# Performance work log

Measured on AMD Instinct MI355X. Metric: run time of the kernel, lower is better.

## Reference

```python
import jax, jax.numpy as jnp
import numpy as np

D_MODEL = 768
HIDDEN = 2048  # round(768*8/3)=2048, already a multiple of 64
N_EXPERTS = 8
ALPHA = 0.05  # load_balance_alpha


def setup_inputs() -> dict:
    key = jax.random.key(0)
    k0, k1, k2, k3, k4 = jax.random.split(key, 5)
    x = jax.random.normal(k0, (2, 2048, D_MODEL), dtype=jnp.float32)
    wg_w = jax.random.normal(k1, (N_EXPERTS, D_MODEL), dtype=jnp.float32) * 0.02
    wg_b = jnp.zeros((N_EXPERTS,), dtype=jnp.float32)
    Wu = jax.random.normal(k2, (N_EXPERTS, D_MODEL, HIDDEN), dtype=jnp.float32) * 0.02
    Wv = jax.random.normal(k3, (N_EXPERTS, D_MODEL, HIDDEN), dtype=jnp.float32) * 0.02
    Wd = jax.random.normal(k4, (N_EXPERTS, HIDDEN, D_MODEL), dtype=jnp.float32) * 0.02
    return {"x": x, "wg_w": wg_w, "wg_b": wg_b, "Wu": Wu, "Wv": Wv, "Wd": Wd}


def reference(x, wg_w, wg_b, Wu, Wv, Wd):
    b, t, d = x.shape
    xf = x.reshape(b * t, d)  # [N, d]

    # ---- Top1Router (eval mode: temp=1, no noise, z_loss_coef=0) ----
    logits = xf @ wg_w.T + wg_b            # [N, E]
    probs = jax.nn.softmax(logits, axis=-1)
    top1_idx = jnp.argmax(logits, axis=-1)  # [N]
    top1_p = jnp.take_along_axis(probs, top1_idx[:, None], axis=1)[:, 0]  # [N]

    # aux loss: me and ce computed under no_grad in the torch source -> stop_gradient
    one_hot = jax.nn.one_hot(top1_idx, N_EXPERTS, dtype=probs.dtype)
    me = jax.lax.stop_gradient(one_hot.mean(axis=0))   # [E]
    ce = jax.lax.stop_gradient(probs.mean(axis=0))     # [E]
    aux = ALPHA * N_EXPERTS * jnp.sum(me * ce)

    # ---- Dropless dispatch: per-expert masked SwiGLU, combined with top1 gate ----
    gate = top1_p[:, None]  # [N, 1]
    y = jnp.zeros_like(xf)
    for e in range(N_EXPERTS):
        mask = (top1_idx == e)[:, None]            # [N, 1]
        xe = jnp.where(mask, xf, 0.0)              # zero-out non-routed tokens (no biases -> exact)
        u = xe @ Wu[e]                              # [N, H]
        v = xe @ Wv[e]                              # [N, H]
        ye = (jax.nn.silu(u) * v) @ Wd[e]           # [N, d]
        y = y + jnp.where(mask, ye * gate, 0.0)
    return y.reshape(b, t, d), aux
```

## Files before the change

### kernel.cpp

```cpp
#include <hip/hip_runtime.h>
#include <cstdint>
#include <cstddef>

#define TOK 4096
#define DM 768
#define HID 2048
#define NE 8

typedef __attribute__((ext_vector_type(8))) short bf16x8;
typedef __attribute__((ext_vector_type(4))) float f32x4;

#define ASYNC16(GP, LP) \
  __builtin_amdgcn_global_load_lds((__attribute__((address_space(1))) void*)(GP), \
                                   (__attribute__((address_space(3))) void*)(LP), 16, 0, 0)

__device__ __forceinline__ unsigned short f2bf(float f) {
  unsigned int u = __float_as_uint(f);
  u += 0x7FFF + ((u >> 16) & 1);
  return (unsigned short)(u >> 16);
}
__device__ __forceinline__ unsigned int pack2(float a, float b) {
  return (unsigned)f2bf(a) | ((unsigned)f2bf(b) << 16);
}
__device__ __forceinline__ int padded_off(const int* counts, int e) {
  int o = 0;
  for (int i = 0; i < e; ++i) o += (counts[i] + 127) & ~127;
  return o;
}

__global__ __launch_bounds__(256)
void k_gate(const float* __restrict__ x, const float* __restrict__ wgw,
            const float* __restrict__ wgb,
            int* __restrict__ eidx, float* __restrict__ gatep,
            float* __restrict__ cepart)
{
  __shared__ float ce_loc[4][NE];
  const int lane = threadIdx.x & 63;
  const int w = threadIdx.x >> 6;
  const int t = blockIdx.x * 4 + w;
  float acc[NE];
#pragma unroll
  for (int e = 0; e < NE; ++e) acc[e] = 0.f;
  const float* xr = x + (size_t)t * DM;
#pragma unroll
  for (int j = 0; j < DM / 64; ++j) {
    float xv = xr[j * 64 + lane];
#pragma unroll
    for (int e = 0; e < NE; ++e) acc[e] += xv * wgw[e * DM + j * 64 + lane];
  }
#pragma unroll
  for (int e = 0; e < NE; ++e) {
    float v = acc[e];
#pragma unroll
    for (int off = 32; off >= 1; off >>= 1) v += __shfl_xor(v, off);
    acc[e] = v + wgb[e];
  }
  float mx = acc[0]; int ai = 0;
#pragma unroll
  for (int e = 1; e < NE; ++e) if (acc[e] > mx) { mx = acc[e]; ai = e; }
  float p[NE]; float se = 0.f;
#pragma unroll
  for (int e = 0; e < NE; ++e) { p[e] = expf(acc[e] - mx); se += p[e]; }
  float inv = 1.f / se;
  if (lane == 0) {
#pragma unroll
    for (int e = 0; e < NE; ++e) ce_loc[w][e] = p[e] * inv;
    eidx[t] = ai;
    gatep[t] = p[ai] * inv;
  }
  __syncthreads();
  if (threadIdx.x < NE) {
    float s = ce_loc[0][threadIdx.x] + ce_loc[1][threadIdx.x]
            + ce_loc[2][threadIdx.x] + ce_loc[3][threadIdx.x];
    cepart[blockIdx.x * NE + threadIdx.x] = s;
  }
}

__global__ __launch_bounds__(256)
void k_convert(const float* __restrict__ Wu, const float* __restrict__ Wv,
               const float* __restrict__ Wd,
               unsigned short* __restrict__ wub, unsigned short* __restrict__ wvb,
               unsigned short* __restrict__ wdb)
{
  const int cb = blockIdx.x;
  const int seg = cb / 1536;
  const int r = cb % 1536;
  const int e = r / 192;
  const int rem = r % 192;
  const float* W;
  unsigned short* blobbase;
  int N, nt, kt2;
  if (seg < 2) {
    N = HID; nt = rem / 12; kt2 = rem % 12;
    W = ((seg == 0) ? Wu : Wv) + (size_t)e * DM * HID;
    blobbase = ((seg == 0) ? wub : wvb) + ((size_t)((e * 16 + nt) * 24) << 12);
  } else {
    N = DM; nt = rem / 32; kt2 = rem % 32;
    W = Wd + (size_t)e * HID * DM;
    blobbase = wdb + ((size_t)((e * 6 + nt) * 64) << 12);
  }
  const int t = threadIdx.x;
  const int n4 = t & 31, ko8 = t >> 5;
  const float* src = W + (size_t)(kt2 * 64 + ko8 * 8) * N + nt * 128 + n4 * 4;
  float4 f[8];
#pragma unroll
  for (int j = 0; j < 8; ++j) f[j] = *(const float4*)(src + (size_t)j * N);
  const int kt = kt2 * 2 + (ko8 >> 2), ko = ko8 & 3;
  unsigned short* dst = blobbase + ((size_t)kt << 12) + (size_t)(ko * 128 + n4 * 4) * 8;
#pragma unroll
  for (int i = 0; i < 4; ++i) {
    uint4 u;
    u.x = pack2(((const float*)&f[0])[i], ((const float*)&f[1])[i]);
    u.y = pack2(((const float*)&f[2])[i], ((const float*)&f[3])[i]);
    u.z = pack2(((const float*)&f[4])[i], ((const float*)&f[5])[i]);
    u.w = pack2(((const float*)&f[6])[i], ((const float*)&f[7])[i]);
    *(uint4*)(dst + i * 8) = u;
  }
}

__global__ __launch_bounds__(256)
void k_count(const int* __restrict__ eidx, const float* __restrict__ gatep,
             const float* __restrict__ cepart,
             int* __restrict__ prow_arr, int* __restrict__ tlist,
             float* __restrict__ gate_b, int* __restrict__ counts_g,
             float* __restrict__ aux_out)
{
  __shared__ int hist[256][NE];
  __shared__ float fs[256][NE];
  __shared__ int po_s[NE], cnt_s[NE];
  const int tid = threadIdx.x;
  int own[NE], v[NE], el[16];
#pragma unroll
  for (int e = 0; e < NE; ++e) own[e] = 0;
#pragma unroll
  for (int j = 0; j < 16; ++j) {
    el[j] = eidx[tid * 16 + j];
#pragma unroll
    for (int e = 0; e < NE; ++e) own[e] += (el[j] == e) ? 1 : 0;
  }
#pragma unroll
  for (int e = 0; e < NE; ++e) { v[e] = own[e]; hist[tid][e] = v[e]; }
  __syncthreads();
  for (int st = 1; st < 256; st <<= 1) {
    int add[NE];
#pragma unroll
    for (int e = 0; e < NE; ++e) add[e] = (tid >= st) ? hist[tid - st][e] : 0;
    __syncthreads();
#pragma unroll
    for (int e = 0; e < NE; ++e) { v[e] += add[e]; hist[tid][e] = v[e]; }
    __syncthreads();
  }
  if (tid == 0) {
    int o = 0;
#pragma unroll
    for (int e = 0; e < NE; ++e) {
      int c = hist[255][e];
      cnt_s[e] = c; counts_g[e] = c; po_s[e] = o;
      o += (c + 127) & ~127;
    }
  }
  __syncthreads();
  int run[NE];
#pragma unroll
  for (int e = 0; e < NE; ++e) run[e] = po_s[e] + v[e] - own[e];
#pragma unroll
  for (int j = 0; j < 16; ++j) {
    const int t = tid * 16 + j;
    const int e = el[j];
    int p = 0;
#pragma unroll
    for (int k = 0; k < NE; ++k) if (e == k) p = run[k]++;
    prow_arr[t] = p;
    tlist[p] = t;
    gate_b[p] = gatep[t];
  }
  float s[NE];
#pragma unroll
  for (int e = 0; e < NE; ++e) s[e] = 0.f;
  for (int bb = tid; bb < 1024; bb += 256)
#pragma unroll
    for (int e = 0; e < NE; ++e) s[e] += cepart[bb * NE + e];
#pragma unroll
  for (int e = 0; e < NE; ++e) fs[tid][e] = s[e];
  __syncthreads();
  for (int st = 128; st > 0; st >>= 1) {
    if (tid < st)
#pragma unroll
      for (int e = 0; e < NE; ++e) fs[tid][e] += fs[tid + st][e];
    __syncthreads();
  }
  if (tid == 0) {
    float aux = 0.f;
    for (int e = 0; e < NE; ++e)
      aux += ((float)cnt_s[e] / 4096.f) * (fs[0][e] / 4096.f);
    aux_out[0] = 0.05f * 8.f * aux;
  }
}

__global__ __launch_bounds__(256)
void k2_scatter_zero(const float* __restrict__ x, const int* __restrict__ prow_arr,
                     unsigned short* __restrict__ xb, float* __restrict__ y)
{
  const int b = blockIdx.x;
  if (b < 1024) {
    const int lane = threadIdx.x & 63;
    const int w = threadIdx.x >> 6;
    const int t = b * 4 + w;
    const int prow = prow_arr[t];
    const float4* src4 = (const float4*)(x + (size_t)t * DM);
    uint2* dst = (uint2*)(xb + (size_t)prow * DM);
#pragma unroll
    for (int c = 0; c < 3; ++c) {
      float4 v = src4[lane + c * 64];
      uint2 d; d.x = pack2(v.x, v.y); d.y = pack2(v.z, v.w);
      dst[lane + c * 64] = d;
    }
  } else {
    float4* y4 = (float4*)y;
    const int base = (b - 1024) * 1536 + threadIdx.x;
#pragma unroll
    for (int c = 0; c < 6; ++c) {
      float4 z; z.x = 0.f; z.y = 0.f; z.z = 0.f; z.w = 0.f;
      y4[base + c * 256] = z;
    }
  }
}

__global__ __launch_bounds__(256, 2)
void k_ffn1(const unsigned short* __restrict__ wub, const unsigned short* __restrict__ wvb,
            const unsigned short* __restrict__ xb, const float* __restrict__ gate_b,
            const int* __restrict__ counts, unsigned short* __restrict__ h)
{
  const int e = blockIdx.z;
  const int Me = counts[e];
  const int tm = blockIdx.y;
  if (tm * 128 >= Me) return;
  const int tn = blockIdx.x;
  const int prowbase = padded_off(counts, e) + tm * 128;

  __shared__ __align__(16) unsigned short Sh[24576];

  const int tid = threadIdx.x;
  const int lane = tid & 63;
  const int wv_ = tid >> 6;
  const int wm = wv_ >> 1, wn = wv_ & 1;
  const int wu_id = __builtin_amdgcn_readfirstlane(wv_);

  f32x4 accU[4][4], accV[4][4];
#pragma unroll
  for (int i = 0; i < 4; ++i)
#pragma unroll
    for (int j = 0; j < 4; ++j)
#pragma unroll
      for (int k = 0; k < 4; ++k) { accU[i][j][k] = 0.f; accV[i][j][k] = 0.f; }

  const char* BuBase = (const char*)wub + ((size_t)((e * 16 + tn) * 24) << 13);
  const char* BvBase = (const char*)wvb + ((size_t)((e * 16 + tn) * 24) << 13);

  const char* sp[12]; size_t stp[12];
#pragma unroll
  for (int c2 = 0; c2 < 12; ++c2) {
    const int c = wu_id * 12 + c2;
    const int reg = c >> 3, i8 = c & 7;
    const int sub = (reg >= 3);
    const int rr = (reg >= 3) ? reg - 3 : reg;
    const int s = i8 * 64 + lane;
    if (rr == 0) {
      int m = s >> 2, ko = (s & 3) ^ (m & 3);
      sp[c2] = (const char*)xb + (size_t)(prowbase + m) * (DM * 2) + sub * 64 + ko * 16;
      stp[c2] = 128;
    } else {
      int n = s >> 2, ko = (s & 3) ^ (n & 3);
      const char* base = (rr == 1) ? BuBase : BvBase;
      sp[c2] = base + (size_t)sub * 8192 + (size_t)(ko * 128 + n) * 16;
      stp[c2] = 16384;
    }
  }
  const int lc = lane & 15, q = lane >> 4;

  for (int kt2 = 0; kt2 < 12; ++kt2) {
#pragma unroll
    for (int c2 = 0; c2 < 12; ++c2) {
      ASYNC16(sp[c2], (char*)Sh + (unsigned)((wu_id * 12 + c2) * 1024));
      sp[c2] += stp[c2];
    }
    __syncthreads();
#pragma unroll
    for (int sub = 0; sub < 2; ++sub) {
      const int sb = sub * 12288;
      bf16x8 a[4], bu[4], bv[4];
#pragma unroll
      for (int i = 0; i < 4; ++i) {
        int m = wm * 64 + i * 16 + lc;
        a[i] = *(const bf16x8*)&Sh[sb + (m * 4 + (q ^ (m & 3))) * 8];
      }
#pragma unroll
      for (int j = 0; j < 4; ++j) {
        int n = wn * 64 + j * 16 + lc;
        int slb = (n * 4 + (q ^ (n & 3))) * 8;
        bu[j] = *(const bf16x8*)&Sh[sb + 4096 + slb];
        bv[j] = *(const bf16x8*)&Sh[sb + 8192 + slb];
      }
#pragma unroll
      for (int i = 0; i < 4; ++i)
#pragma unroll
        for (int j = 0; j < 4; ++j) {
          accU[i][j] = __builtin_amdgcn_mfma_f32_16x16x32_bf16(a[i], bu[j], accU[i][j], 0, 0, 0);
          accV[i][j] = __builtin_amdgcn_mfma_f32_16x16x32_bf16(a[i], bv[j], accV[i][j], 0, 0, 0);
        }
    }
    __syncthreads();
  }
  const int colbase = tn * 128 + wn * 64;
  const int rlane = (lane >> 4) * 4;
  const int clane = lane & 15;
#pragma unroll
  for (int i = 0; i < 4; ++i) {
#pragma unroll
    for (int r = 0; r < 4; ++r) {
      int rowIn = wm * 64 + i * 16 + rlane + r;
      if (tm * 128 + rowIn < Me) {
        int prow = prowbase + rowIn;
        float g = gate_b[prow];
        unsigned short* hp = h + (size_t)prow * HID + colbase + clane;
#pragma unroll
        for (int j = 0; j < 4; ++j) {
          float u_ = accU[i][j][r];
          float v_ = accV[i][j][r];
          float sv = u_ / (1.f + expf(-u_));
          hp[j * 16] = f2bf(sv * v_ * g);
        }
      }
    }
  }
}

__global__ __launch_bounds__(256, 2)
void k_ffn2(const unsigned short* __restrict__ wdb, const unsigned short* __restrict__ h,
            const int* __restrict__ counts, const int* __restrict__ tlist,
            float* __restrict__ y)
{
  const int z = blockIdx.z;
  const int e = z >> 2, split = z & 3;
  const int Me = counts[e];
  const int tm = blockIdx.y;
  if (tm * 128 >= Me) return;
  const int tn = blockIdx.x;
  const int prowbase = padded_off(counts, e) + tm * 128;

  __shared__ __align__(16) unsigned short Sh[16384];

  const int tid = threadIdx.x;
  const int lane = tid & 63;
  const int wv_ = tid >> 6;
  const int wm = wv_ >> 1, wn = wv_ & 1;
  const int wu_id = __builtin_amdgcn_readfirstlane(wv_);

  f32x4 acc[4][4];
#pragma unroll
  for (int i = 0; i < 4; ++i)
#pragma unroll
    for (int j = 0; j < 4; ++j)
#pragma unroll
      for (int k = 0; k < 4; ++k) acc[i][j][k] = 0.f;

  const char* BdBase = (const char*)wdb + ((size_t)((e * 6 + tn) * 64) << 13);

  const char* sp[8]; size_t stp[8];
#pragma unroll
  for (int c2 = 0; c2 < 8; ++c2) {
    const int c = wu_id * 8 + c2;
    const int reg = c >> 3, i8 = c & 7;
    const int sub = reg >> 1;
    const int s = i8 * 64 + lane;
    if ((reg & 1) == 0) {
      int m = s >> 2, ko = (s & 3) ^ (m & 3);
      sp[c2] = (const char*)h + (size_t)(prowbase + m) * (HID * 2)
             + split * 1024 + sub * 64 + ko * 16;
      stp[c2] = 128;
    } else {
      int n = s >> 2, ko = (s & 3) ^ (n & 3);
      sp[c2] = BdBase + (size_t)(split * 16 + sub) * 8192 + (size_t)(ko * 128 + n) * 16;
      stp[c2] = 16384;
    }
  }
  const int lc = lane & 15, q = lane >> 4;

  for (int kti = 0; kti < 8; ++kti) {
#pragma unroll
    for (int c2 = 0; c2 < 8; ++c2) {
      ASYNC16(sp[c2], (char*)Sh + (unsigned)((wu_id * 8 + c2) * 1024));
      sp[c2] += stp[c2];
    }
    __syncthreads();
#pragma unroll
    for (int sub = 0; sub < 2; ++sub) {
      const int sb = sub * 8192;
      bf16x8 a[4], bfr[4];
#pragma unroll
      for (int i = 0; i < 4; ++i) {
        int m = wm * 64 + i * 16 + lc;
        a[i] = *(const bf16x8*)&Sh[sb + (m * 4 + (q ^ (m & 3))) * 8];
      }
#pragma unroll
      for (int j = 0; j < 4; ++j) {
        int n = wn * 64 + j * 16 + lc;
        bfr[j] = *(const bf16x8*)&Sh[sb + 4096 + (n * 4 + (q ^ (n & 3))) * 8];
      }
#pragma unroll
      for (int i = 0; i < 4; ++i)
#pragma unroll
        for (int j = 0; j < 4; ++j)
          acc[i][j] = __builtin_amdgcn_mfma_f32_16x16x32_bf16(a[i], bfr[j], acc[i][j], 0, 0, 0);
    }
    __syncthreads();
  }
  const int colbase = tn * 128 + wn * 64;
  const int rlane = (lane >> 4) * 4;
  const int clane = lane & 15;
#pragma unroll
  for (int i = 0; i < 4; ++i) {
#pragma unroll
    for (int r = 0; r < 4; ++r) {
      int rowIn = wm * 64 + i * 16 + rlane + r;
      if (tm * 128 + rowIn < Me) {
        int tok = tlist[prowbase + rowIn];
        float* yp = y + (size_t)tok * DM + colbase + clane;
#pragma unroll
        for (int j = 0; j < 4; ++j) atomicAdd(&yp[j * 16], acc[i][j][r]);
      }
    }
  }
}

extern "C" void kernel_launch(void* const* d_in, const int* in_sizes, int n_in,
                              void* d_out, int out_size, void* d_ws, size_t ws_size,
                              hipStream_t stream)
{
  const float* x   = (const float*)d_in[0];
  const float* wgw = (const float*)d_in[1];
  const float* wgb = (const float*)d_in[2];
  const float* Wu  = (const float*)d_in[3];
  const float* Wv  = (const float*)d_in[4];
  const float* Wd  = (const float*)d_in[5];
  float* out = (float*)d_out;

  char* ws = (char*)d_ws;
  int*   counts = (int*)(ws + 0);
  int*   eidx   = (int*)(ws + 256);
  float* gatep  = (float*)(ws + 16640);
  int*   prow   = (int*)(ws + 33024);
  float* cepart = (float*)(ws + 49408);
  int*   tlist  = (int*)(ws + 82176);
  float* gate_b = (float*)(ws + 102656);
  unsigned short* xb  = (unsigned short*)(ws + 123136);
  unsigned short* h   = (unsigned short*)(ws + 7987456);
  unsigned short* wub = (unsigned short*)(ws + 28958976);
  unsigned short* wvb = (unsigned short*)(ws + 54124800);
  unsigned short* wdb = (unsigned short*)(ws + 79290624);

  k_gate<<<1024, 256, 0, stream>>>(x, wgw, wgb, eidx, gatep, cepart);
  k_convert<<<4608, 256, 0, stream>>>(Wu, Wv, Wd, wub, wvb, wdb);
  k_count<<<1, 256, 0, stream>>>(eidx, gatep, cepart, prow, tlist, gate_b,
                                 counts, out + (size_t)TOK * DM);
  k2_scatter_zero<<<1536, 256, 0, stream>>>(x, prow, xb, out);
  k_ffn1<<<dim3(16, 32, 8), 256, 0, stream>>>(wub, wvb, xb, gate_b, counts, h);
  k_ffn2<<<dim3(6, 32, 32), 256, 0, stream>>>(wdb, h, counts, tlist, out);
}
```

Measured before the change: 343.8 us.

## Fuse fp32-to-bf16 weight conversion into FFN kernels with double-buffered LDS

Removes the separate weight-conversion kernel; the FFN kernels now read fp32 expert weights directly, pack them to bf16 in registers and write them into LDS. The kernels switch to 512 threads with 256-row M tiles, double-buffered shared memory where the next tile's loads overlap the current MFMAs, and a flattened grid with expert as the fastest index. This avoids writing and re-reading a bf16 copy of all weights, but each block now reads fp32 weights (twice the bytes) and weights are re-read once per M tile, with register-staged loads that may stall.

```diff
diff --git a/kernel.cpp b/kernel.cpp
--- a/kernel.cpp
+++ b/kernel.cpp
@@ -73,48 +73,6 @@
     float s = ce_loc[0][threadIdx.x] + ce_loc[1][threadIdx.x]
             + ce_loc[2][threadIdx.x] + ce_loc[3][threadIdx.x];
     cepart[blockIdx.x * NE + threadIdx.x] = s;
-  }
-}
-
-__global__ __launch_bounds__(256)
-void k_convert(const float* __restrict__ Wu, const float* __restrict__ Wv,
-               const float* __restrict__ Wd,
-               unsigned short* __restrict__ wub, unsigned short* __restrict__ wvb,
-               unsigned short* __restrict__ wdb)
-{
-  const int cb = blockIdx.x;
-  const int seg = cb / 1536;
-  const int r = cb % 1536;
-  const int e = r / 192;
-  const int rem = r % 192;
-  const float* W;
-  unsigned short* blobbase;
-  int N, nt, kt2;
-  if (seg < 2) {
-    N = HID; nt = rem / 12; kt2 = rem % 12;
-    W = ((seg == 0) ? Wu : Wv) + (size_t)e * DM * HID;
-    blobbase = ((seg == 0) ? wub : wvb) + ((size_t)((e * 16 + nt) * 24) << 12);
-  } else {
-    N = DM; nt = rem / 32; kt2 = rem % 32;
-    W = Wd + (size_t)e * HID * DM;
-    blobbase = wdb + ((size_t)((e * 6 + nt) * 64) << 12);
-  }
-  const int t = threadIdx.x;
-  const int n4 = t & 31, ko8 = t >> 5;
-  const float* src = W + (size_t)(kt2 * 64 + ko8 * 8) * N + nt * 128 + n4 * 4;
-  float4 f[8];
-#pragma unroll
-  for (int j = 0; j < 8; ++j) f[j] = *(const float4*)(src + (size_t)j * N);
-  const int kt = kt2 * 2 + (ko8 >> 2), ko = ko8 & 3;
-  unsigned short* dst = blobbase + ((size_t)kt << 12) + (size_t)(ko * 128 + n4 * 4) * 8;
-#pragma unroll
-  for (int i = 0; i < 4; ++i) {
-    uint4 u;
-    u.x = pack2(((const float*)&f[0])[i], ((const float*)&f[1])[i]);
-    u.y = pack2(((const float*)&f[2])[i], ((const float*)&f[3])[i]);
-    u.z = pack2(((const float*)&f[4])[i], ((const float*)&f[5])[i]);
-    u.w = pack2(((const float*)&f[6])[i], ((const float*)&f[7])[i]);
-    *(uint4*)(dst + i * 8) = u;
   }
 }
 
@@ -226,25 +184,53 @@
   }
 }
 
-__global__ __launch_bounds__(256, 2)
-void k_ffn1(const unsigned short* __restrict__ wub, const unsigned short* __restrict__ wvb,
+__global__ __launch_bounds__(512, 2)
+void k_ffn1(const float* __restrict__ Wu, const float* __restrict__ Wv,
             const unsigned short* __restrict__ xb, const float* __restrict__ gate_b,
             const int* __restrict__ counts, unsigned short* __restrict__ h)
 {
-  const int e = blockIdx.z;
+  const int bid = blockIdx.x;
+  const int e = bid & 7;
+  const int r_ = bid >> 3;
+  const int tm = r_ & 15;
+  const int tn = r_ >> 4;
   const int Me = counts[e];
-  const int tm = blockIdx.y;
-  if (tm * 128 >= Me) return;
-  const int tn = blockIdx.x;
-  const int prowbase = padded_off(counts, e) + tm * 128;
-
-  __shared__ __align__(16) unsigned short Sh[24576];
+  if (tm * 256 >= Me) return;
+  const int prowbase = padded_off(counts, e) + tm * 256;
+
+  __shared__ __align__(16) char Sh[65536];
 
   const int tid = threadIdx.x;
   const int lane = tid & 63;
-  const int wv_ = tid >> 6;
-  const int wm = wv_ >> 1, wn = wv_ & 1;
-  const int wu_id = __builtin_amdgcn_readfirstlane(wv_);
+  const int w = tid >> 6;
+  const int wm = w >> 1, wn = w & 1;
+
+  const int c0 = w * 2, c1 = w * 2 + 1;
+  const int mA0 = c0 * 16 + (lane >> 2), sA0 = lane & 3;
+  const int ko0 = (sA0 - mA0 - (mA0 >> 2)) & 3;
+  const char* aSrc0 = (const char*)xb + (size_t)(prowbase + mA0) * (DM * 2) + ko0 * 16;
+  const int mA1 = c1 * 16 + (lane >> 2), sA1 = lane & 3;
+  const int ko1 = (sA1 - mA1 - (mA1 >> 2)) & 3;
+  const char* aSrc1 = (const char*)xb + (size_t)(prowbase + mA1) * (DM * 2) + ko1 * 16;
+
+  const int koW = w & 3;
+  const int nloc = (w >> 2) * 64 + lane;
+  const unsigned offBw = (unsigned)(nloc * 4 + ((koW + nloc + (nloc >> 2)) & 3)) * 16;
+  const int ncol = tn * 128 + nloc;
+  const float* srcU = Wu + (size_t)e * DM * HID + (size_t)(koW * 8) * HID + ncol;
+  const float* srcV = Wv + (size_t)e * DM * HID + (size_t)(koW * 8) * HID + ncol;
+
+  const int lc = lane & 15, q = lane >> 4;
+  unsigned offA[4], offU[4], offV[4];
+#pragma unroll
+  for (int i = 0; i < 4; ++i) {
+    int m = wm * 64 + i * 16 + lc;
+    offA[i] = (unsigned)(m * 4 + ((q + m + (m >> 2)) & 3)) * 16;
+    int n = wn * 64 + i * 16 + lc;
+    unsigned ob = (unsigned)(n * 4 + ((q + n + (n >> 2)) & 3)) * 16;
+    offU[i] = 16384u + ob;
+    offV[i] = 24576u + ob;
+  }
 
   f32x4 accU[4][4], accV[4][4];
 #pragma unroll
@@ -254,79 +240,77 @@
 #pragma unroll
       for (int k = 0; k < 4; ++k) { accU[i][j][k] = 0.f; accV[i][j][k] = 0.f; }
 
-  const char* BuBase = (const char*)wub + ((size_t)((e * 16 + tn) * 24) << 13);
-  const char* BvBase = (const char*)wvb + ((size_t)((e * 16 + tn) * 24) << 13);
-
-  const char* sp[12]; size_t stp[12];
-#pragma unroll
-  for (int c2 = 0; c2 < 12; ++c2) {
-    const int c = wu_id * 12 + c2;
-    const int reg = c >> 3, i8 = c & 7;
-    const int sub = (reg >= 3);
-    const int rr = (reg >= 3) ? reg - 3 : reg;
-    const int s = i8 * 64 + lane;
-    if (rr == 0) {
-      int m = s >> 2, ko = (s & 3) ^ (m & 3);
-      sp[c2] = (const char*)xb + (size_t)(prowbase + m) * (DM * 2) + sub * 64 + ko * 16;
-      stp[c2] = 128;
-    } else {
-      int n = s >> 2, ko = (s & 3) ^ (n & 3);
-      const char* base = (rr == 1) ? BuBase : BvBase;
-      sp[c2] = base + (size_t)sub * 8192 + (size_t)(ko * 128 + n) * 16;
-      stp[c2] = 16384;
-    }
-  }
-  const int lc = lane & 15, q = lane >> 4;
-
-  for (int kt2 = 0; kt2 < 12; ++kt2) {
-#pragma unroll
-    for (int c2 = 0; c2 < 12; ++c2) {
-      ASYNC16(sp[c2], (char*)Sh + (unsigned)((wu_id * 12 + c2) * 1024));
-      sp[c2] += stp[c2];
+  float fu[8], fv[8];
+  ASYNC16(aSrc0, Sh + c0 * 1024); aSrc0 += 64;
+  ASYNC16(aSrc1, Sh + c1 * 1024); aSrc1 += 64;
+#pragma unroll
+  for (int j = 0; j < 8; ++j) { fu[j] = srcU[(size_t)j * HID]; fv[j] = srcV[(size_t)j * HID]; }
+  srcU += (size_t)32 * HID; srcV += (size_t)32 * HID;
+  {
+    uint4 up, vp;
+    up.x = pack2(fu[0], fu[1]); up.y = pack2(fu[2], fu[3]);
+    up.z = pack2(fu[4], fu[5]); up.w = pack2(fu[6], fu[7]);
+    vp.x = pack2(fv[0], fv[1]); vp.y = pack2(fv[2], fv[3]);
+    vp.z = pack2(fv[4], fv[5]); vp.w = pack2(fv[6], fv[7]);
+    *(uint4*)(Sh + 16384 + offBw) = up;
+    *(uint4*)(Sh + 24576 + offBw) = vp;
+  }
+  __syncthreads();
+
+  for (int kt = 0; kt < 24; ++kt) {
+    char* bufc = Sh + (unsigned)(kt & 1) * 32768u;
+    char* bufn = Sh + (unsigned)((kt + 1) & 1) * 32768u;
+    const bool more = (kt + 1) < 24;
+    if (more) {
+      ASYNC16(aSrc0, bufn + c0 * 1024); aSrc0 += 64;
+      ASYNC16(aSrc1, bufn + c1 * 1024); aSrc1 += 64;
+#pragma unroll
+      for (int j = 0; j < 8; ++j) { fu[j] = srcU[(size_t)j * HID]; fv[j] = srcV[(size_t)j * HID]; }
+      srcU += (size_t)32 * HID; srcV += (size_t)32 * HID;
+    }
+    bf16x8 a[4], bu[4], bv[4];
+#pragma unroll
+    for (int i = 0; i < 4; ++i) a[i] = *(const bf16x8*)(bufc + offA[i]);
+#pragma unroll
+    for (int j = 0; j < 4; ++j) {
+      bu[j] = *(const bf16x8*)(bufc + offU[j]);
+      bv[j] = *(const bf16x8*)(bufc + offV[j]);
+    }
+#pragma unroll
+    for (int i = 0; i < 4; ++i)
+#pragma unroll
+      for (int j = 0; j < 4; ++j) {
+        accU[i][j] = __builtin_amdgcn_mfma_f32_16x16x32_bf16(a[i], bu[j], accU[i][j], 0, 0, 0);
+        accV[i][j] = __builtin_amdgcn_mfma_f32_16x16x32_bf16(a[i], bv[j], accV[i][j], 0, 0, 0);
+      }
+    if (more) {
+      uint4 up, vp;
+      up.x = pack2(fu[0], fu[1]); up.y = pack2(fu[2], fu[3]);
+      up.z = pack2(fu[4], fu[5]); up.w = pack2(fu[6], fu[7]);
+      vp.x = pack2(fv[0], fv[1]); vp.y = pack2(fv[2], fv[3]);
+      vp.z = pack2(fv[4], fv[5]); vp.w = pack2(fv[6], fv[7]);
+      *(uint4*)(bufn + 16384 + offBw) = up;
+      *(uint4*)(bufn + 24576 + offBw) = vp;
     }
     __syncthreads();
-#pragma unroll
-    for (int sub = 0; sub < 2; ++sub) {
-      const int sb = sub * 12288;
-      bf16x8 a[4], bu[4], bv[4];
-#pragma unroll
-      for (int i = 0; i < 4; ++i) {
-        int m = wm * 64 + i * 16 + lc;
-        a[i] = *(const bf16x8*)&Sh[sb + (m * 4 + (q ^ (m & 3))) * 8];
-      }
-#pragma unroll
-      for (int j = 0; j < 4; ++j) {
-        int n = wn * 64 + j * 16 + lc;
-        int slb = (n * 4 + (q ^ (n & 3))) * 8;
-        bu[j] = *(const bf16x8*)&Sh[sb + 4096 + slb];
-        bv[j] = *(const bf16x8*)&Sh[sb + 8192 + slb];
-      }
-#pragma unroll
-      for (int i = 0; i < 4; ++i)
-#pragma unroll
-        for (int j = 0; j < 4; ++j) {
-          accU[i][j] = __builtin_amdgcn_mfma_f32_16x16x32_bf16(a[i], bu[j], accU[i][j], 0, 0, 0);
-          accV[i][j] = __builtin_amdgcn_mfma_f32_16x16x32_bf16(a[i], bv[j], accV[i][j], 0, 0, 0);
-        }
-    }
-    __syncthreads();
-  }
+  }
+
   const int colbase = tn * 128 + wn * 64;
   const int rlane = (lane >> 4) * 4;
   const int clane = lane & 15;
 #pragma unroll
   for (int i = 0; i < 4; ++i) {
 #pragma unroll
-    for (int r = 0; r < 4; ++r) {
-      int rowIn = wm * 64 + i * 16 + rlane + r;
-      if (tm * 128 + rowIn < Me) {
+    for (int rr = 0; rr < 4; ++rr) {
+      int rowIn = wm * 64 + i * 16 + rlane + rr;
+      if (tm * 256 + rowIn < Me) {
         int prow = prowbase + rowIn;
         float g = gate_b[prow];
         unsigned short* hp = h + (size_t)prow * HID + colbase + clane;
 #pragma unroll
         for (int j = 0; j < 4; ++j) {
-          float u_ = accU[i][j][r];
-          float v_ = accV[i][j][r];
+          float u_ = accU[i][j][rr];
+          float v_ = accV[i][j][rr];
           float sv = u_ / (1.f + expf(-u_));
           hp[j * 16] = f2bf(sv * v_ * g);
         }
@@ -335,26 +319,51 @@
   }
 }
 
-__global__ __launch_bounds__(256, 2)
-void k_ffn2(const unsigned short* __restrict__ wdb, const unsigned short* __restrict__ h,
+__global__ __launch_bounds__(512, 2)
+void k_ffn2(const float* __restrict__ Wd, const unsigned short* __restrict__ h,
             const int* __restrict__ counts, const int* __restrict__ tlist,
             float* __restrict__ y)
 {
-  const int z = blockIdx.z;
-  const int e = z >> 2, split = z & 3;
+  const int bid = blockIdx.x;
+  const int e = bid & 7;
+  int r_ = bid >> 3;
+  const int tn = r_ % 6; r_ /= 6;
+  const int sk = r_ & 3;
+  const int tm = r_ >> 2;
   const int Me = counts[e];
-  const int tm = blockIdx.y;
-  if (tm * 128 >= Me) return;
-  const int tn = blockIdx.x;
-  const int prowbase = padded_off(counts, e) + tm * 128;
-
-  __shared__ __align__(16) unsigned short Sh[16384];
+  if (tm * 256 >= Me) return;
+  const int prowbase = padded_off(counts, e) + tm * 256;
+
+  __shared__ __align__(16) char Sh[49152];
 
   const int tid = threadIdx.x;
   const int lane = tid & 63;
-  const int wv_ = tid >> 6;
-  const int wm = wv_ >> 1, wn = wv_ & 1;
-  const int wu_id = __builtin_amdgcn_readfirstlane(wv_);
+  const int w = tid >> 6;
+  const int wm = w >> 1, wn = w & 1;
+
+  const int c0 = w * 2, c1 = w * 2 + 1;
+  const int mA0 = c0 * 16 + (lane >> 2), sA0 = lane & 3;
+  const int ko0 = (sA0 - mA0 - (mA0 >> 2)) & 3;
+  const char* aSrc0 = (const char*)h + (size_t)(prowbase + mA0) * (HID * 2) + sk * 1024 + ko0 * 16;
+  const int mA1 = c1 * 16 + (lane >> 2), sA1 = lane & 3;
+  const int ko1 = (sA1 - mA1 - (mA1 >> 2)) & 3;
+  const char* aSrc1 = (const char*)h + (size_t)(prowbase + mA1) * (HID * 2) + sk * 1024 + ko1 * 16;
+
+  const int nloc = tid & 127;
+  const int koW = tid >> 7;
+  const unsigned offBw = (unsigned)(nloc * 4 + ((koW + nloc + (nloc >> 2)) & 3)) * 16;
+  const int ncol = tn * 128 + nloc;
+  const float* srcD = Wd + (size_t)e * HID * DM + (size_t)(sk * 512 + koW * 8) * DM + ncol;
+
+  const int lc = lane & 15, q = lane >> 4;
+  unsigned offA[4], offBr[4];
+#pragma unroll
+  for (int i = 0; i < 4; ++i) {
+    int m = wm * 64 + i * 16 + lc;
+    offA[i] = (unsigned)(m * 4 + ((q + m + (m >> 2)) & 3)) * 16;
+    int n = wn * 64 + i * 16 + lc;
+    offBr[i] = 16384u + (unsigned)(n * 4 + ((q + n + (n >> 2)) & 3)) * 16;
+  }
 
   f32x4 acc[4][4];
 #pragma unroll
@@ -364,70 +373,63 @@
 #pragma unroll
       for (int k = 0; k < 4; ++k) acc[i][j][k] = 0.f;
 
-  const char* BdBase = (const char*)wdb + ((size_t)((e * 6 + tn) * 64) << 13);
-
-  const char* sp[8]; size_t stp[8];
-#pragma unroll
-  for (int c2 = 0; c2 < 8; ++c2) {
-    const int c = wu_id * 8 + c2;
-    const int reg = c >> 3, i8 = c & 7;
-    const int sub = reg >> 1;
-    const int s = i8 * 64 + lane;
-    if ((reg & 1) == 0) {
-      int m = s >> 2, ko = (s & 3) ^ (m & 3);
-      sp[c2] = (const char*)h + (size_t)(prowbase + m) * (HID * 2)
-             + split * 1024 + sub * 64 + ko * 16;
-      stp[c2] = 128;
-    } else {
-      int n = s >> 2, ko = (s & 3) ^ (n & 3);
-      sp[c2] = BdBase + (size_t)(split * 16 + sub) * 8192 + (size_t)(ko * 128 + n) * 16;
-      stp[c2] = 16384;
-    }
-  }
-  const int lc = lane & 15, q = lane >> 4;
-
-  for (int kti = 0; kti < 8; ++kti) {
-#pragma unroll
-    for (int c2 = 0; c2 < 8; ++c2) {
-      ASYNC16(sp[c2], (char*)Sh + (unsigned)((wu_id * 8 + c2) * 1024));
-      sp[c2] += stp[c2];
+  float fd[8];
+  ASYNC16(aSrc0, Sh + c0 * 1024); aSrc0 += 64;
+  ASYNC16(aSrc1, Sh + c1 * 1024); aSrc1 += 64;
+#pragma unroll
+  for (int j = 0; j < 8; ++j) fd[j] = srcD[(size_t)j * DM];
+  srcD += (size_t)32 * DM;
+  {
+    uint4 dp;
+    dp.x = pack2(fd[0], fd[1]); dp.y = pack2(fd[2], fd[3]);
+    dp.z = pack2(fd[4], fd[5]); dp.w = pack2(fd[6], fd[7]);
+    *(uint4*)(Sh + 16384 + offBw) = dp;
+  }
+  __syncthreads();
+
+  for (int kt = 0; kt < 16; ++kt) {
+    char* bufc = Sh + (unsigned)(kt & 1) * 24576u;
+    char* bufn = Sh + (unsigned)((kt + 1) & 1) * 24576u;
+    const bool more = (kt + 1) < 16;
+    if (more) {
+      ASYNC16(aSrc0, bufn + c0 * 1024); aSrc0 += 64;
+      ASYNC16(aSrc1, bufn + c1 * 1024); aSrc1 += 64;
+#pragma unroll
+      for (int j = 0; j < 8; ++j) fd[j] = srcD[(size_t)j * DM];
+      srcD += (size_t)32 * DM;
+    }
+    bf16x8 a[4], b[4];
+#pragma unroll
+    for (int i = 0; i < 4; ++i) a[i] = *(const bf16x8*)(bufc + offA[i]);
+#pragma unroll
+    for (int j = 0; j < 4; ++j) b[j] = *(const bf16x8*)(bufc + offBr[j]);
+#pragma unroll
+    for (int i = 0; i < 4; ++i)
+#pragma unroll
+      for (int j = 0; j < 4; ++j)
+        acc[i][j] = __builtin_amdgcn_mfma_f32_16x16x32_bf16(a[i], b[j], acc[i][j], 0, 0, 0);
+    if (more) {
+      uint4 dp;
+      dp.x = pack2(fd[0], fd[1]); dp.y = pack2(fd[2], fd[3]);
+      dp.z = pack2(fd[4], fd[5]); dp.w = pack2(fd[6], fd[7]);
+      *(uint4*)(bufn + 16384 + offBw) = dp;
     }
     __syncthreads();
-#pragma unroll
-    for (int sub = 0; sub < 2; ++sub) {
-      const int sb = sub * 8192;
-      bf16x8 a[4], bfr[4];
-#pragma unroll
-      for (int i = 0; i < 4; ++i) {
-        int m = wm * 64 + i * 16 + lc;
-        a[i] = *(const bf16x8*)&Sh[sb + (m * 4 + (q ^ (m & 3))) * 8];
-      }
-#pragma unroll
-      for (int j = 0; j < 4; ++j) {
-        int n = wn * 64 + j * 16 + lc;
-        bfr[j] = *(const bf16x8*)&Sh[sb + 4096 + (n * 4 + (q ^ (n & 3))) * 8];
-      }
-#pragma unroll
-      for (int i = 0; i < 4; ++i)
-#pragma unroll
-        for (int j = 0; j < 4; ++j)
-          acc[i][j] = __builtin_amdgcn_mfma_f32_16x16x32_bf16(a[i], bfr[j], acc[i][j], 0, 0, 0);
-    }
-    __syncthreads();
-  }
+  }
+
   const int colbase = tn * 128 + wn * 64;
   const int rlane = (lane >> 4) * 4;
   const int clane = lane & 15;
 #pragma unroll
   for (int i = 0; i < 4; ++i) {
 #pragma unroll
-    for (int r = 0; r < 4; ++r) {
-      int rowIn = wm * 64 + i * 16 + rlane + r;
-      if (tm * 128 + rowIn < Me) {
+    for (int rr = 0; rr < 4; ++rr) {
+      int rowIn = wm * 64 + i * 16 + rlane + rr;
+      if (tm * 256 + rowIn < Me) {
         int tok = tlist[prowbase + rowIn];
         float* yp = y + (size_t)tok * DM + colbase + clane;
 #pragma unroll
-        for (int j = 0; j < 4; ++j) atomicAdd(&yp[j * 16], acc[i][j][r]);
+        for (int j = 0; j < 4; ++j) atomicAdd(&yp[j * 16], acc[i][j][rr]);
       }
     }
   }
@@ -455,15 +457,11 @@
   float* gate_b = (float*)(ws + 102656);
   unsigned short* xb  = (unsigned short*)(ws + 123136);
   unsigned short* h   = (unsigned short*)(ws + 7987456);
-  unsigned short* wub = (unsigned short*)(ws + 28958976);
-  unsigned short* wvb = (unsigned short*)(ws + 54124800);
-  unsigned short* wdb = (unsigned short*)(ws + 79290624);
 
   k_gate<<<1024, 256, 0, stream>>>(x, wgw, wgb, eidx, gatep, cepart);
-  k_convert<<<4608, 256, 0, stream>>>(Wu, Wv, Wd, wub, wvb, wdb);
   k_count<<<1, 256, 0, stream>>>(eidx, gatep, cepart, prow, tlist, gate_b,
                                  counts, out + (size_t)TOK * DM);
   k2_scatter_zero<<<1536, 256, 0, stream>>>(x, prow, xb, out);
-  k_ffn1<<<dim3(16, 32, 8), 256, 0, stream>>>(wub, wvb, xb, gate_b, counts, h);
-  k_ffn2<<<dim3(6, 32, 32), 256, 0, stream>>>(wdb, h, counts, tlist, out);
-}
+  k_ffn1<<<2048, 512, 0, stream>>>(Wu, Wv, xb, gate_b, counts, h);
+  k_ffn2<<<3072, 512, 0, stream>>>(Wd, h, counts, tlist, out);
+}
```

Result: slower. 363.4 us (+5.7%).

## Drop split-K in down projection, store directly; merge gate and weight-convert kernels

Applied to the files above, without the earlier changes.

Merges the gating and weight-conversion kernels into one launch. Removes the 4-way split-K in the down-projection GEMM, so each block covers the full hidden dimension and writes outputs with plain stores. This drops the atomicAdds and the pass that zeroed y. Since every token goes to exactly one expert, each output row is written once. The cost is four times fewer blocks and a longer K loop in the second GEMM, which may leave the GPU underfilled.

```diff
diff --git a/kernel.cpp b/kernel.cpp
--- a/kernel.cpp
+++ b/kernel.cpp
@@ -29,92 +29,92 @@
 }
 
 __global__ __launch_bounds__(256)
-void k_gate(const float* __restrict__ x, const float* __restrict__ wgw,
-            const float* __restrict__ wgb,
-            int* __restrict__ eidx, float* __restrict__ gatep,
-            float* __restrict__ cepart)
+void k_pre(const float* __restrict__ x, const float* __restrict__ wgw,
+           const float* __restrict__ wgb,
+           const float* __restrict__ Wu, const float* __restrict__ Wv,
+           const float* __restrict__ Wd,
+           int* __restrict__ eidx, float* __restrict__ gatep,
+           float* __restrict__ cepart,
+           unsigned short* __restrict__ wub, unsigned short* __restrict__ wvb,
+           unsigned short* __restrict__ wdb)
 {
   __shared__ float ce_loc[4][NE];
-  const int lane = threadIdx.x & 63;
-  const int w = threadIdx.x >> 6;
-  const int t = blockIdx.x * 4 + w;
-  float acc[NE];
-#pragma unroll
-  for (int e = 0; e < NE; ++e) acc[e] = 0.f;
-  const float* xr = x + (size_t)t * DM;
-#pragma unroll
-  for (int j = 0; j < DM / 64; ++j) {
-    float xv = xr[j * 64 + lane];
-#pragma unroll
-    for (int e = 0; e < NE; ++e) acc[e] += xv * wgw[e * DM + j * 64 + lane];
-  }
-#pragma unroll
-  for (int e = 0; e < NE; ++e) {
-    float v = acc[e];
-#pragma unroll
-    for (int off = 32; off >= 1; off >>= 1) v += __shfl_xor(v, off);
-    acc[e] = v + wgb[e];
-  }
-  float mx = acc[0]; int ai = 0;
-#pragma unroll
-  for (int e = 1; e < NE; ++e) if (acc[e] > mx) { mx = acc[e]; ai = e; }
-  float p[NE]; float se = 0.f;
-#pragma unroll
-  for (int e = 0; e < NE; ++e) { p[e] = expf(acc[e] - mx); se += p[e]; }
-  float inv = 1.f / se;
-  if (lane == 0) {
-#pragma unroll
-    for (int e = 0; e < NE; ++e) ce_loc[w][e] = p[e] * inv;
-    eidx[t] = ai;
-    gatep[t] = p[ai] * inv;
-  }
-  __syncthreads();
-  if (threadIdx.x < NE) {
-    float s = ce_loc[0][threadIdx.x] + ce_loc[1][threadIdx.x]
-            + ce_loc[2][threadIdx.x] + ce_loc[3][threadIdx.x];
-    cepart[blockIdx.x * NE + threadIdx.x] = s;
-  }
-}
-
-__global__ __launch_bounds__(256)
-void k_convert(const float* __restrict__ Wu, const float* __restrict__ Wv,
-               const float* __restrict__ Wd,
-               unsigned short* __restrict__ wub, unsigned short* __restrict__ wvb,
-               unsigned short* __restrict__ wdb)
-{
-  const int cb = blockIdx.x;
-  const int seg = cb / 1536;
-  const int r = cb % 1536;
-  const int e = r / 192;
-  const int rem = r % 192;
-  const float* W;
-  unsigned short* blobbase;
-  int N, nt, kt2;
-  if (seg < 2) {
-    N = HID; nt = rem / 12; kt2 = rem % 12;
-    W = ((seg == 0) ? Wu : Wv) + (size_t)e * DM * HID;
-    blobbase = ((seg == 0) ? wub : wvb) + ((size_t)((e * 16 + nt) * 24) << 12);
+  const int b = blockIdx.x;
+  if (b < 1024) {
+    const int lane = threadIdx.x & 63;
+    const int w = threadIdx.x >> 6;
+    const int t = b * 4 + w;
+    float acc[NE];
+#pragma unroll
+    for (int e = 0; e < NE; ++e) acc[e] = 0.f;
+    const float* xr = x + (size_t)t * DM;
+#pragma unroll
+    for (int j = 0; j < DM / 64; ++j) {
+      float xv = xr[j * 64 + lane];
+#pragma unroll
+      for (int e = 0; e < NE; ++e) acc[e] += xv * wgw[e * DM + j * 64 + lane];
+    }
+#pragma unroll
+    for (int e = 0; e < NE; ++e) {
+      float v = acc[e];
+#pragma unroll
+      for (int off = 32; off >= 1; off >>= 1) v += __shfl_xor(v, off);
+      acc[e] = v + wgb[e];
+    }
+    float mx = acc[0]; int ai = 0;
+#pragma unroll
+    for (int e = 1; e < NE; ++e) if (acc[e] > mx) { mx = acc[e]; ai = e; }
+    float p[NE]; float se = 0.f;
+#pragma unroll
+    for (int e = 0; e < NE; ++e) { p[e] = expf(acc[e] - mx); se += p[e]; }
+    float inv = 1.f / se;
+    if (lane == 0) {
+#pragma unroll
+      for (int e = 0; e < NE; ++e) ce_loc[w][e] = p[e] * inv;
+      eidx[t] = ai;
+      gatep[t] = p[ai] * inv;
+    }
+    __syncthreads();
+    if (threadIdx.x < NE) {
+      float s = ce_loc[0][threadIdx.x] + ce_loc[1][threadIdx.x]
+              + ce_loc[2][threadIdx.x] + ce_loc[3][threadIdx.x];
+      cepart[b * NE + threadIdx.x] = s;
+    }
   } else {
-    N = DM; nt = rem / 32; kt2 = rem % 32;
-    W = Wd + (size_t)e * HID * DM;
-    blobbase = wdb + ((size_t)((e * 6 + nt) * 64) << 12);
-  }
-  const int t = threadIdx.x;
-  const int n4 = t & 31, ko8 = t >> 5;
-  const float* src = W + (size_t)(kt2 * 64 + ko8 * 8) * N + nt * 128 + n4 * 4;
-  float4 f[8];
-#pragma unroll
-  for (int j = 0; j < 8; ++j) f[j] = *(const float4*)(src + (size_t)j * N);
-  const int kt = kt2 * 2 + (ko8 >> 2), ko = ko8 & 3;
-  unsigned short* dst = blobbase + ((size_t)kt << 12) + (size_t)(ko * 128 + n4 * 4) * 8;
-#pragma unroll
-  for (int i = 0; i < 4; ++i) {
-    uint4 u;
-    u.x = pack2(((const float*)&f[0])[i], ((const float*)&f[1])[i]);
-    u.y = pack2(((const float*)&f[2])[i], ((const float*)&f[3])[i]);
-    u.z = pack2(((const float*)&f[4])[i], ((const float*)&f[5])[i]);
-    u.w = pack2(((const float*)&f[6])[i], ((const float*)&f[7])[i]);
-    *(uint4*)(dst + i * 8) = u;
+    const int cb = b - 1024;
+    const int seg = cb / 1536;
+    const int r = cb % 1536;
+    const int e = r / 192;
+    const int rem = r % 192;
+    const float* W;
+    unsigned short* blobbase;
+    int N, nt, kt2;
+    if (seg < 2) {
+      N = HID; nt = rem / 12; kt2 = rem % 12;
+      W = ((seg == 0) ? Wu : Wv) + (size_t)e * DM * HID;
+      blobbase = ((seg == 0) ? wub : wvb) + ((size_t)((e * 16 + nt) * 24) << 12);
+    } else {
+      N = DM; nt = rem / 32; kt2 = rem % 32;
+      W = Wd + (size_t)e * HID * DM;
+      blobbase = wdb + ((size_t)((e * 6 + nt) * 64) << 12);
+    }
+    const int t = threadIdx.x;
+    const int n4 = t & 31, ko8 = t >> 5;
+    const float* src = W + (size_t)(kt2 * 64 + ko8 * 8) * N + nt * 128 + n4 * 4;
+    float4 f[8];
+#pragma unroll
+    for (int j = 0; j < 8; ++j) f[j] = *(const float4*)(src + (size_t)j * N);
+    const int kt = kt2 * 2 + (ko8 >> 2), ko = ko8 & 3;
+    unsigned short* dst = blobbase + ((size_t)kt << 12) + (size_t)(ko * 128 + n4 * 4) * 8;
+#pragma unroll
+    for (int i = 0; i < 4; ++i) {
+      uint4 u;
+      u.x = pack2(((const float*)&f[0])[i], ((const float*)&f[1])[i]);
+      u.y = pack2(((const float*)&f[2])[i], ((const float*)&f[3])[i]);
+      u.z = pack2(((const float*)&f[4])[i], ((const float*)&f[5])[i]);
+      u.w = pack2(((const float*)&f[6])[i], ((const float*)&f[7])[i]);
+      *(uint4*)(dst + i * 8) = u;
+    }
   }
 }
 
@@ -198,31 +198,21 @@
 }
 
 __global__ __launch_bounds__(256)
-void k2_scatter_zero(const float* __restrict__ x, const int* __restrict__ prow_arr,
-                     unsigned short* __restrict__ xb, float* __restrict__ y)
+void k2_scatter(const float* __restrict__ x, const int* __restrict__ prow_arr,
+                unsigned short* __restrict__ xb)
 {
   const int b = blockIdx.x;
-  if (b < 1024) {
-    const int lane = threadIdx.x & 63;
-    const int w = threadIdx.x >> 6;
-    const int t = b * 4 + w;
-    const int prow = prow_arr[t];
-    const float4* src4 = (const float4*)(x + (size_t)t * DM);
-    uint2* dst = (uint2*)(xb + (size_t)prow * DM);
-#pragma unroll
-    for (int c = 0; c < 3; ++c) {
-      float4 v = src4[lane + c * 64];
-      uint2 d; d.x = pack2(v.x, v.y); d.y = pack2(v.z, v.w);
-      dst[lane + c * 64] = d;
-    }
-  } else {
-    float4* y4 = (float4*)y;
-    const int base = (b - 1024) * 1536 + threadIdx.x;
-#pragma unroll
-    for (int c = 0; c < 6; ++c) {
-      float4 z; z.x = 0.f; z.y = 0.f; z.z = 0.f; z.w = 0.f;
-      y4[base + c * 256] = z;
-    }
+  const int lane = threadIdx.x & 63;
+  const int w = threadIdx.x >> 6;
+  const int t = b * 4 + w;
+  const int prow = prow_arr[t];
+  const float4* src4 = (const float4*)(x + (size_t)t * DM);
+  uint2* dst = (uint2*)(xb + (size_t)prow * DM);
+#pragma unroll
+  for (int c = 0; c < 3; ++c) {
+    float4 v = src4[lane + c * 64];
+    uint2 d; d.x = pack2(v.x, v.y); d.y = pack2(v.z, v.w);
+    dst[lane + c * 64] = d;
   }
 }
 
@@ -340,8 +330,7 @@
             const int* __restrict__ counts, const int* __restrict__ tlist,
             float* __restrict__ y)
 {
-  const int z = blockIdx.z;
-  const int e = z >> 2, split = z & 3;
+  const int e = blockIdx.z;
   const int Me = counts[e];
   const int tm = blockIdx.y;
   if (tm * 128 >= Me) return;
@@ -376,17 +365,17 @@
     if ((reg & 1) == 0) {
       int m = s >> 2, ko = (s & 3) ^ (m & 3);
       sp[c2] = (const char*)h + (size_t)(prowbase + m) * (HID * 2)
-             + split * 1024 + sub * 64 + ko * 16;
+             + sub * 64 + ko * 16;
       stp[c2] = 128;
     } else {
       int n = s >> 2, ko = (s & 3) ^ (n & 3);
-      sp[c2] = BdBase + (size_t)(split * 16 + sub) * 8192 + (size_t)(ko * 128 + n) * 16;
+      sp[c2] = BdBase + (size_t)sub * 8192 + (size_t)(ko * 128 + n) * 16;
       stp[c2] = 16384;
     }
   }
   const int lc = lane & 15, q = lane >> 4;
 
-  for (int kti = 0; kti < 8; ++kti) {
+  for (int kti = 0; kti < 32; ++kti) {
 #pragma unroll
     for (int c2 = 0; c2 < 8; ++c2) {
       ASYNC16(sp[c2], (char*)Sh + (unsigned)((wu_id * 8 + c2) * 1024));
@@ -427,7 +416,7 @@
         int tok = tlist[prowbase + rowIn];
         float* yp = y + (size_t)tok * DM + colbase + clane;
 #pragma unroll
-        for (int j = 0; j < 4; ++j) atomicAdd(&yp[j * 16], acc[i][j][r]);
+        for (int j = 0; j < 4; ++j) yp[j * 16] = acc[i][j][r];
       }
     }
   }
@@ -459,11 +448,11 @@
   unsigned short* wvb = (unsigned short*)(ws + 54124800);
   unsigned short* wdb = (unsigned short*)(ws + 79290624);
 
-  k_gate<<<1024, 256, 0, stream>>>(x, wgw, wgb, eidx, gatep, cepart);
-  k_convert<<<4608, 256, 0, stream>>>(Wu, Wv, Wd, wub, wvb, wdb);
+  k_pre<<<1024 + 4608, 256, 0, stream>>>(x, wgw, wgb, Wu, Wv, Wd,
+                                         eidx, gatep, cepart, wub, wvb, wdb);
   k_count<<<1, 256, 0, stream>>>(eidx, gatep, cepart, prow, tlist, gate_b,
                                  counts, out + (size_t)TOK * DM);
-  k2_scatter_zero<<<1536, 256, 0, stream>>>(x, prow, xb, out);
+  k2_scatter<<<1024, 256, 0, stream>>>(x, prow, xb);
   k_ffn1<<<dim3(16, 32, 8), 256, 0, stream>>>(wub, wvb, xb, gate_b, counts, h);
-  k_ffn2<<<dim3(6, 32, 32), 256, 0, stream>>>(wdb, h, counts, tlist, out);
-}
+  k_ffn2<<<dim3(6, 32, 8), 256, 0, stream>>>(wdb, h, counts, tlist, out);
+}
```

New measurement: 346.9 us. About the same (+0.9%).
